# Optimization experiments

Measured on AMD Instinct MI355X. Metric: run time of the kernel, lower is better.

Reference implementation:

```python
import jax, jax.numpy as jnp
import numpy as np

GROUP_SIZE = 64  # int4 precision
QMAX = 7.0       # symmetric int4 quant scale divisor


def setup_inputs() -> dict:
    key = jax.random.key(0)
    ks = jax.random.split(key, 8)
    B, S, C_in, C_out, R = 1, 4096, 3072, 3072, 32
    G = C_in // GROUP_SIZE
    x = jax.random.normal(ks[0], (B, S, C_in), dtype=jnp.float32)
    # unpacked int4 weight codes in [0,16); reference subtracts 8 -> signed int4 [-8,7]
    qweight = jax.random.randint(ks[1], (C_out, C_in), 0, 16, dtype=jnp.int32)
    # small positive per-group, per-out-channel weight scales
    wscales = jax.random.uniform(ks[2], (G, C_out), dtype=jnp.float32) * 0.01 + 0.001
    # positive smoothing factors bounded away from zero
    smooth_factor = jax.random.uniform(ks[3], (C_in,), dtype=jnp.float32) + 0.5
    proj_down = jax.random.normal(ks[4], (C_in, R), dtype=jnp.float32) * (1.0 / np.sqrt(C_in))
    proj_up = jax.random.normal(ks[5], (C_out, R), dtype=jnp.float32) * (1.0 / np.sqrt(R))
    bias = jax.random.normal(ks[6], (C_out,), dtype=jnp.float32) * 0.02
    return {
        "x": x,
        "qweight": qweight,
        "wscales": wscales,
        "smooth_factor": smooth_factor,
        "proj_down": proj_down,
        "proj_up": proj_up,
        "bias": bias,
    }


def reference(x, qweight, wscales, smooth_factor, proj_down, proj_up, bias):
    B, S, C = x.shape
    C_out = qweight.shape[0]
    M = B * S
    G = C // GROUP_SIZE

    # --- smoothing: x_hat = x / s (SVDQuant smoothing on activations) ---
    xs = x.reshape(M, C) / smooth_factor  # (M, C)

    # --- low-rank branch hidden state (fused with quantization in CUDA kernel) ---
    lora_act = jnp.einsum('mc,cr->mr', xs, proj_down)  # (M, R)

    # --- dynamic per-token, per-group int4 activation quantization ---
    xg = xs.reshape(M, G, GROUP_SIZE)
    amax = jnp.max(jnp.abs(xg), axis=-1, keepdims=True)          # (M, G, 1)
    ascale = amax / QMAX
    q = jnp.clip(jnp.round(xg / jnp.maximum(ascale, 1e-8)), -8.0, 7.0)
    x_dq = (q * ascale).reshape(M, C)                            # dequantized activations

    # --- weight dequantization: signed int4 codes * per-group/out-channel scales ---
    qw = qweight.astype(jnp.float32) - 8.0                       # (C_out, C) in [-8, 7]
    w_dq = (qw.reshape(C_out, G, GROUP_SIZE) * wscales.T[:, :, None]).reshape(C_out, C)

    # --- quantized GEMM + low-rank correction + bias ---
    out = jnp.einsum('mc,oc->mo', x_dq, w_dq)
    out = out + jnp.einsum('mr,or->mo', lora_act, proj_up) + bias
    return out.reshape(B, S, C_out)
```

## Files before the change

kernel.cpp:

```cpp
#include <hip/hip_runtime.h>
#include <stdint.h>

typedef unsigned short u16;

#define MTOK 4096
#define CIN  3072
#define COUT 3072
#define RANK 32
#define KT48 48
#define RS   3136
#define LKSPLIT 16
#define LKC (CIN/LKSPLIT)

#define LORA_BLK (MTOK/128*LKSPLIT)
#define WDQ_BLK COUT


typedef __attribute__((ext_vector_type(8))) short bf16x8;
typedef __attribute__((ext_vector_type(4))) float f32x4;

__device__ __forceinline__ u16 f2bf(float f) {
  union { float f; unsigned u; } v; v.f = f;
  unsigned r = v.u + 0x7FFFu + ((v.u >> 16) & 1u);
  return (u16)(r >> 16);
}

__device__ __forceinline__ void gload_lds16(const void* g, void* l) {
  __builtin_amdgcn_global_load_lds(
      (const __attribute__((address_space(1))) unsigned int*)g,
      (__attribute__((address_space(3))) unsigned int*)l, 16, 0, 0);
}

__device__ __forceinline__ float quant1(float xs, float ascale, float qd) {
  float q = rintf(xs / qd);
  q = fminf(fmaxf(q, -8.f), 7.f);
  return q * ascale;
}

__global__ __launch_bounds__(256) void prep_kernel(
    const float* __restrict__ x, const float* __restrict__ smooth,
    const int* __restrict__ qw, const float* __restrict__ wsc,
    const float* __restrict__ pd, const float* __restrict__ pu,
    u16* __restrict__ xdq, u16* __restrict__ wdq, u16* __restrict__ pu_bf,
    float* __restrict__ lp)
{
  const int b = blockIdx.x;
  const int t = threadIdx.x;

  if (b < LORA_BLK) {
    __shared__ __align__(16) u16 sA[128 * 64];
    __shared__ __align__(16) u16 sB[32 * 64];
    const int m0 = (b >> 4) * 128;
    const int kblk = b & 15;
    const int wave = t >> 6, lane = t & 63;
    const int lm = lane & 15, lkq = (lane >> 4) * 8;

    f32x4 acc[2][2];
    const f32x4 fz = {0.f, 0.f, 0.f, 0.f};
#pragma unroll
    for (int i = 0; i < 2; ++i)
#pragma unroll
      for (int j = 0; j < 2; ++j) acc[i][j] = fz;

    for (int kt = 0; kt < LKC / 64; ++kt) {
      const int k0 = kblk * LKC + kt * 64;
      const int col = (t & 15) * 4;
#pragma unroll
      for (int it = 0; it < 8; ++it) {
        const int row = it * 16 + (t >> 4);
        const float4 xv = *(const float4*)(x + (size_t)(m0 + row) * CIN + k0 + col);
        const float4 sv = *(const float4*)(smooth + k0 + col);
        const float xs0 = xv.x / sv.x, xs1 = xv.y / sv.y;
        const float xs2 = xv.z / sv.z, xs3 = xv.w / sv.w;
        ushort4 ov;
        ov.x = f2bf(xs0); ov.y = f2bf(xs1); ov.z = f2bf(xs2); ov.w = f2bf(xs3);
        *(ushort4*)&sA[row * 64 + col] = ov;
        float a = fmaxf(fmaxf(fabsf(xs0), fabsf(xs1)), fmaxf(fabsf(xs2), fabsf(xs3)));
#pragma unroll
        for (int off = 1; off < 16; off <<= 1) a = fmaxf(a, __shfl_xor(a, off));
        const float ascale = a / 7.0f;
        const float qd = fmaxf(ascale, 1e-8f);
        ushort4 oq;
        oq.x = f2bf(quant1(xs0, ascale, qd));
        oq.y = f2bf(quant1(xs1, ascale, qd));
        oq.z = f2bf(quant1(xs2, ascale, qd));
        oq.w = f2bf(quant1(xs3, ascale, qd));
        *(ushort4*)(xdq + (size_t)(m0 + row) * RS + k0 + col) = oq;
      }
#pragma unroll
      for (int i = 0; i < 8; ++i) {
        const int idx = i * 256 + t;
        const int k = idx >> 5, r = idx & 31;
        sB[r * 64 + k] = f2bf(pd[(size_t)(k0 + k) * RANK + r]);
      }
      __syncthreads();
#pragma unroll
      for (int kk = 0; kk < 2; ++kk) {
        const int ko = kk * 32 + lkq;
        bf16x8 af[2], bfr[2];
#pragma unroll
        for (int i = 0; i < 2; ++i)
          af[i] = *(const bf16x8*)&sA[(wave * 32 + i * 16 + lm) * 64 + ko];
#pragma unroll
        for (int j = 0; j < 2; ++j)
          bfr[j] = *(const bf16x8*)&sB[(j * 16 + lm) * 64 + ko];
#pragma unroll
        for (int i = 0; i < 2; ++i)
#pragma unroll
          for (int j = 0; j < 2; ++j)
            acc[i][j] = __builtin_amdgcn_mfma_f32_16x16x32_bf16(af[i], bfr[j], acc[i][j], 0, 0, 0);
      }
      __syncthreads();
    }
    float* lpk = lp + (size_t)kblk * MTOK * RANK;
#pragma unroll
    for (int i = 0; i < 2; ++i)
#pragma unroll
      for (int j = 0; j < 2; ++j) {
        const int col = j * 16 + lm;
        const int row0 = m0 + wave * 32 + i * 16 + (lane >> 4) * 4;
#pragma unroll
        for (int r = 0; r < 4; ++r)
          lpk[(size_t)(row0 + r) * RANK + col] = acc[i][j][r];
      }
  } else {
    const int o = b - LORA_BLK;
    const int4* qrow = (const int4*)(qw + (size_t)o * CIN);
    u16* orow = wdq + (size_t)o * RS;
#pragma unroll
    for (int p = 0; p < 3; ++p) {
      const int c4 = p * 256 + t;
      const int g = (c4 * 4) >> 6;
      const float ws = wsc[g * COUT + o];
      const int4 qv = qrow[c4];
      ushort4 ov;
      ov.x = f2bf((float)(qv.x - 8) * ws);
      ov.y = f2bf((float)(qv.y - 8) * ws);
      ov.z = f2bf((float)(qv.z - 8) * ws);
      ov.w = f2bf((float)(qv.w - 8) * ws);
      ((ushort4*)orow)[c4] = ov;
    }
    if (t < RANK) pu_bf[(size_t)o * RANK + t] = f2bf(pu[(size_t)o * RANK + t]);
  }
}

__global__ __launch_bounds__(256) void lora_fix_kernel(
    const float* __restrict__ lp, u16* __restrict__ lora_bf)
{
  const int idx = blockIdx.x * 256 + threadIdx.x;
  const int m = idx >> 5, c = idx & 31;
  float s = 0.f;
#pragma unroll
  for (int k = 0; k < LKSPLIT; ++k) s += lp[((size_t)k * MTOK + m) * RANK + c];
  lora_bf[(size_t)m * RANK + c] = f2bf(s);
}

__global__ __launch_bounds__(256) void gemm_kernel(
    const u16* __restrict__ xdq, const u16* __restrict__ wdq,
    const u16* __restrict__ pu_bf, const u16* __restrict__ lora_bf,
    const float* __restrict__ bias, float* __restrict__ out)
{
  __shared__ __align__(16) u16 sA[128 * 64];
  __shared__ __align__(16) u16 sB[128 * 64];
  const int t = threadIdx.x;
  const int wave = t >> 6, lane = t & 63;
  const int wm = wave >> 1, wn = wave & 1;
  const int m0 = blockIdx.y * 128, n0 = blockIdx.x * 128;
  const int lrow = lane >> 3;
  const int gcol = ((lane & 7) ^ lrow) * 8;

  f32x4 acc[4][4];
  const f32x4 fz = {0.f, 0.f, 0.f, 0.f};
#pragma unroll
  for (int i = 0; i < 4; ++i)
#pragma unroll
    for (int j = 0; j < 4; ++j) acc[i][j] = fz;

  const int lm = lane & 15;
  const int xs7 = lm & 7;
  const int q4 = lane >> 4;

  for (int kt = 0; kt < KT48; ++kt) {
    const u16* Ab = xdq + (size_t)m0 * RS + kt * 64;
    const u16* Bb = wdq + (size_t)n0 * RS + kt * 64;
#pragma unroll
    for (int r = 0; r < 4; ++r) {
      const int ci = wave * 4 + r;
      const int row = ci * 8 + lrow;
      gload_lds16(Ab + (size_t)row * RS + gcol, &sA[ci * 512 + lane * 8]);
      gload_lds16(Bb + (size_t)row * RS + gcol, &sB[ci * 512 + lane * 8]);
    }
    __syncthreads();
#pragma unroll
    for (int kk = 0; kk < 2; ++kk) {
      const int csw = ((kk * 4 + q4) ^ xs7) * 8;
      bf16x8 af[4], bfr[4];
#pragma unroll
      for (int i = 0; i < 4; ++i)
        af[i] = *(const bf16x8*)&sA[(wm * 64 + i * 16 + lm) * 64 + csw];
#pragma unroll
      for (int j = 0; j < 4; ++j)
        bfr[j] = *(const bf16x8*)&sB[(wn * 64 + j * 16 + lm) * 64 + csw];
#pragma unroll
      for (int i = 0; i < 4; ++i)
#pragma unroll
        for (int j = 0; j < 4; ++j)
          acc[i][j] = __builtin_amdgcn_mfma_f32_16x16x32_bf16(af[i], bfr[j], acc[i][j], 0, 0, 0);
    }
    __syncthreads();
  }

  bf16x8 afl[4], bfl[4];
#pragma unroll
  for (int i = 0; i < 4; ++i) {
    const int arow = m0 + wm * 64 + i * 16 + lm;
    afl[i] = *(const bf16x8*)(lora_bf + (size_t)arow * RANK + q4 * 8);
  }
#pragma unroll
  for (int j = 0; j < 4; ++j) {
    const int bcol = n0 + wn * 64 + j * 16 + lm;
    bfl[j] = *(const bf16x8*)(pu_bf + (size_t)bcol * RANK + q4 * 8);
  }
#pragma unroll
  for (int i = 0; i < 4; ++i)
#pragma unroll
    for (int j = 0; j < 4; ++j)
      acc[i][j] = __builtin_amdgcn_mfma_f32_16x16x32_bf16(afl[i], bfl[j], acc[i][j], 0, 0, 0);

#pragma unroll
  for (int j = 0; j < 4; ++j) {
    const int col = n0 + wn * 64 + j * 16 + lm;
    const float bv = bias[col];
#pragma unroll
    for (int i = 0; i < 4; ++i) {
      const int row0 = m0 + wm * 64 + i * 16 + (lane >> 4) * 4;
#pragma unroll
      for (int r = 0; r < 4; ++r)
        out[(size_t)(row0 + r) * COUT + col] = acc[i][j][r] + bv;
    }
  }
}

extern "C" void kernel_launch(void* const* d_in, const int* in_sizes, int n_in,
                              void* d_out, int out_size, void* d_ws, size_t ws_size,
                              hipStream_t stream) {
  const float* x      = (const float*)d_in[0];
  const int*   qw     = (const int*)d_in[1];
  const float* wsc    = (const float*)d_in[2];
  const float* smooth = (const float*)d_in[3];
  const float* pd     = (const float*)d_in[4];
  const float* pu     = (const float*)d_in[5];
  const float* bias   = (const float*)d_in[6];
  float* out = (float*)d_out;

  u16* xdq     = (u16*)d_ws;
  u16* wdq     = xdq + (size_t)MTOK * RS;
  u16* pu_bf   = wdq + (size_t)COUT * RS;
  u16* lora_bf = pu_bf + (size_t)COUT * RANK;
  float* lp    = (float*)(lora_bf + (size_t)MTOK * RANK);

  prep_kernel<<<LORA_BLK + WDQ_BLK, 256, 0, stream>>>(
      x, smooth, qw, wsc, pd, pu, xdq, wdq, pu_bf, lp);
  lora_fix_kernel<<<MTOK * RANK / 256, 256, 0, stream>>>(lp, lora_bf);
  gemm_kernel<<<dim3(COUT / 128, MTOK / 128), 256, 0, stream>>>(
      xdq, wdq, pu_bf, lora_bf, bias, out);
}
```

Measured before the change: 256.2 us.

## Split activation quantization into streaming kernel and feed LoRA via async LDS loads

Moves smoothing and int4 quantization out of the LoRA-down blocks into a separate fully parallel quant kernel that also writes a bf16 copy of the smoothed activations and a transposed bf16 proj_down. The LoRA blocks then load both operands straight into LDS with global_load_lds and an XOR swizzle, instead of doing per-element divides and strided scalar proj_down loads inside a small grid. This aims to raise parallelism in the quantization pass and remove the scalar transpose work. The cost is an extra kernel launch plus writing and re-reading an extra bf16 activation buffer.

After: 265.2 us. 1.04x slower.

```diff
diff --git a/kernel.cpp b/kernel.cpp
--- a/kernel.cpp
+++ b/kernel.cpp
@@ -12,6 +12,8 @@
 #define LKSPLIT 16
 #define LKC (CIN/LKSPLIT)
 
+#define QBLK (MTOK*3)
+#define PDT_BLK 24
 #define LORA_BLK (MTOK/128*LKSPLIT)
 #define WDQ_BLK COUT
 
@@ -37,12 +39,56 @@
   return q * ascale;
 }
 
-__global__ __launch_bounds__(256) void prep_kernel(
+__global__ __launch_bounds__(256) void quant_kernel(
     const float* __restrict__ x, const float* __restrict__ smooth,
+    const float* __restrict__ pd,
+    u16* __restrict__ xdq, u16* __restrict__ xs_bf, u16* __restrict__ pdT_bf)
+{
+  const int b = blockIdx.x;
+  const int t = threadIdx.x;
+  if (b < QBLK) {
+    const int m = b / 3;
+    const int part = b - m * 3;
+    const int c0 = part * 1024 + t * 4;
+    const float4 xv = *(const float4*)(x + (size_t)m * CIN + c0);
+    const float4 sv = *(const float4*)(smooth + c0);
+    const float xs0 = xv.x / sv.x, xs1 = xv.y / sv.y;
+    const float xs2 = xv.z / sv.z, xs3 = xv.w / sv.w;
+    ushort4 osb;
+    osb.x = f2bf(xs0); osb.y = f2bf(xs1); osb.z = f2bf(xs2); osb.w = f2bf(xs3);
+    *(ushort4*)(xs_bf + (size_t)m * RS + c0) = osb;
+    float a = fmaxf(fmaxf(fabsf(xs0), fabsf(xs1)), fmaxf(fabsf(xs2), fabsf(xs3)));
+#pragma unroll
+    for (int off = 1; off < 16; off <<= 1) a = fmaxf(a, __shfl_xor(a, off));
+    const float ascale = a / 7.0f;
+    const float qd = fmaxf(ascale, 1e-8f);
+    ushort4 oq;
+    oq.x = f2bf(quant1(xs0, ascale, qd));
+    oq.y = f2bf(quant1(xs1, ascale, qd));
+    oq.z = f2bf(quant1(xs2, ascale, qd));
+    oq.w = f2bf(quant1(xs3, ascale, qd));
+    *(ushort4*)(xdq + (size_t)m * RS + c0) = oq;
+  } else {
+    const int k0 = (b - QBLK) * 128;
+    const int k = k0 + (t >> 3);
+    const int r4 = (t & 7) * 4;
+#pragma unroll
+    for (int kp = 0; kp < 4; ++kp) {
+      const int kk = k + kp * 32;
+      const float4 pv = *(const float4*)(pd + (size_t)kk * RANK + r4);
+      pdT_bf[(size_t)(r4 + 0) * CIN + kk] = f2bf(pv.x);
+      pdT_bf[(size_t)(r4 + 1) * CIN + kk] = f2bf(pv.y);
+      pdT_bf[(size_t)(r4 + 2) * CIN + kk] = f2bf(pv.z);
+      pdT_bf[(size_t)(r4 + 3) * CIN + kk] = f2bf(pv.w);
+    }
+  }
+}
+
+__global__ __launch_bounds__(256) void lora_wdq_kernel(
+    const u16* __restrict__ xs_bf, const u16* __restrict__ pdT_bf,
     const int* __restrict__ qw, const float* __restrict__ wsc,
-    const float* __restrict__ pd, const float* __restrict__ pu,
-    u16* __restrict__ xdq, u16* __restrict__ wdq, u16* __restrict__ pu_bf,
-    float* __restrict__ lp)
+    const float* __restrict__ pu,
+    u16* __restrict__ wdq, u16* __restrict__ pu_bf, float* __restrict__ lp)
 {
   const int b = blockIdx.x;
   const int t = threadIdx.x;
@@ -53,7 +99,10 @@
     const int m0 = (b >> 4) * 128;
     const int kblk = b & 15;
     const int wave = t >> 6, lane = t & 63;
-    const int lm = lane & 15, lkq = (lane >> 4) * 8;
+    const int lm = lane & 15, q4 = lane >> 4;
+    const int xs7 = lm & 7;
+    const int lrow = lane >> 3;
+    const int gcol = ((lane & 7) ^ lrow) * 8;
 
     f32x4 acc[2][2];
     const f32x4 fz = {0.f, 0.f, 0.f, 0.f};
@@ -64,46 +113,29 @@
 
     for (int kt = 0; kt < LKC / 64; ++kt) {
       const int k0 = kblk * LKC + kt * 64;
-      const int col = (t & 15) * 4;
-#pragma unroll
-      for (int it = 0; it < 8; ++it) {
-        const int row = it * 16 + (t >> 4);
-        const float4 xv = *(const float4*)(x + (size_t)(m0 + row) * CIN + k0 + col);
-        const float4 sv = *(const float4*)(smooth + k0 + col);
-        const float xs0 = xv.x / sv.x, xs1 = xv.y / sv.y;
-        const float xs2 = xv.z / sv.z, xs3 = xv.w / sv.w;
-        ushort4 ov;
-        ov.x = f2bf(xs0); ov.y = f2bf(xs1); ov.z = f2bf(xs2); ov.w = f2bf(xs3);
-        *(ushort4*)&sA[row * 64 + col] = ov;
-        float a = fmaxf(fmaxf(fabsf(xs0), fabsf(xs1)), fmaxf(fabsf(xs2), fabsf(xs3)));
-#pragma unroll
-        for (int off = 1; off < 16; off <<= 1) a = fmaxf(a, __shfl_xor(a, off));
-        const float ascale = a / 7.0f;
-        const float qd = fmaxf(ascale, 1e-8f);
-        ushort4 oq;
-        oq.x = f2bf(quant1(xs0, ascale, qd));
-        oq.y = f2bf(quant1(xs1, ascale, qd));
-        oq.z = f2bf(quant1(xs2, ascale, qd));
-        oq.w = f2bf(quant1(xs3, ascale, qd));
-        *(ushort4*)(xdq + (size_t)(m0 + row) * RS + k0 + col) = oq;
+#pragma unroll
+      for (int r = 0; r < 4; ++r) {
+        const int ci = wave * 4 + r;
+        const int row = ci * 8 + lrow;
+        gload_lds16(xs_bf + (size_t)(m0 + row) * RS + k0 + gcol,
+                    &sA[ci * 512 + lane * 8]);
       }
-#pragma unroll
-      for (int i = 0; i < 8; ++i) {
-        const int idx = i * 256 + t;
-        const int k = idx >> 5, r = idx & 31;
-        sB[r * 64 + k] = f2bf(pd[(size_t)(k0 + k) * RANK + r]);
+      {
+        const int row = wave * 8 + lrow;
+        gload_lds16(pdT_bf + (size_t)row * CIN + k0 + gcol,
+                    &sB[wave * 512 + lane * 8]);
       }
       __syncthreads();
 #pragma unroll
       for (int kk = 0; kk < 2; ++kk) {
-        const int ko = kk * 32 + lkq;
+        const int csw = ((kk * 4 + q4) ^ xs7) * 8;
         bf16x8 af[2], bfr[2];
 #pragma unroll
         for (int i = 0; i < 2; ++i)
-          af[i] = *(const bf16x8*)&sA[(wave * 32 + i * 16 + lm) * 64 + ko];
+          af[i] = *(const bf16x8*)&sA[(wave * 32 + i * 16 + lm) * 64 + csw];
 #pragma unroll
         for (int j = 0; j < 2; ++j)
-          bfr[j] = *(const bf16x8*)&sB[(j * 16 + lm) * 64 + ko];
+          bfr[j] = *(const bf16x8*)&sB[(j * 16 + lm) * 64 + csw];
 #pragma unroll
         for (int i = 0; i < 2; ++i)
 #pragma unroll
@@ -118,7 +150,7 @@
 #pragma unroll
       for (int j = 0; j < 2; ++j) {
         const int col = j * 16 + lm;
-        const int row0 = m0 + wave * 32 + i * 16 + (lane >> 4) * 4;
+        const int row0 = m0 + wave * 32 + i * 16 + q4 * 4;
 #pragma unroll
         for (int r = 0; r < 4; ++r)
           lpk[(size_t)(row0 + r) * RANK + col] = acc[i][j][r];
@@ -233,7 +265,7 @@
     const float bv = bias[col];
 #pragma unroll
     for (int i = 0; i < 4; ++i) {
-      const int row0 = m0 + wm * 64 + i * 16 + (lane >> 4) * 4;
+      const int row0 = m0 + wm * 64 + i * 16 + q4 * 4;
 #pragma unroll
       for (int r = 0; r < 4; ++r)
         out[(size_t)(row0 + r) * COUT + col] = acc[i][j][r] + bv;
@@ -255,12 +287,15 @@
 
   u16* xdq     = (u16*)d_ws;
   u16* wdq     = xdq + (size_t)MTOK * RS;
-  u16* pu_bf   = wdq + (size_t)COUT * RS;
+  u16* xs_bf   = wdq + (size_t)COUT * RS;
+  u16* pdT_bf  = xs_bf + (size_t)MTOK * RS;
+  u16* pu_bf   = pdT_bf + (size_t)RANK * CIN;
   u16* lora_bf = pu_bf + (size_t)COUT * RANK;
   float* lp    = (float*)(lora_bf + (size_t)MTOK * RANK);
 
-  prep_kernel<<<LORA_BLK + WDQ_BLK, 256, 0, stream>>>(
-      x, smooth, qw, wsc, pd, pu, xdq, wdq, pu_bf, lp);
+  quant_kernel<<<QBLK + PDT_BLK, 256, 0, stream>>>(x, smooth, pd, xdq, xs_bf, pdT_bf);
+  lora_wdq_kernel<<<LORA_BLK + WDQ_BLK, 256, 0, stream>>>(
+      xs_bf, pdT_bf, qw, wsc, pu, wdq, pu_bf, lp);
   lora_fix_kernel<<<MTOK * RANK / 256, 256, 0, stream>>>(lp, lora_bf);
   gemm_kernel<<<dim3(COUT / 128, MTOK / 128), 256, 0, stream>>>(
       xdq, wdq, pu_bf, lora_bf, bias, out);
```
